# Optimization experiments

Hardware: AMD Instinct MI355X
Metric: run time of the kernel (lower is better)

## Reference

```python
import jax, jax.numpy as jnp
import numpy as np

B, T, N = 256, 2048, 64
START_IDX, END_IDX = 1, 2  # mead Offsets.GO, Offsets.EOS
NEG_INF = -10000.0


def setup_inputs() -> dict:
    key = jax.random.key(0)
    k1, k2, k3 = jax.random.split(key, 3)
    unary = jax.random.normal(k1, (B, T, N), dtype=jnp.float32)
    trans = jax.random.normal(k2, (N, N), dtype=jnp.float32) * 0.1  # [to_tag, from_tag]
    lengths = jax.random.randint(k3, (B,), T // 2, T + 1, dtype=jnp.int32)
    return {"unary": unary, "trans": trans, "lengths": lengths}


def reference(unary, trans, lengths):
    """CRF forward algorithm (partition function), batch_first input.

    unary: [B, T, N] emission scores
    trans: [N, N]    trans[j, k] = score of transitioning from tag k to tag j
    lengths: [B]     valid sequence lengths
    returns: [B]     log partition scores
    """
    unary_tbn = jnp.transpose(unary, (1, 0, 2))  # [T, B, N]
    n_tags = trans.shape[0]

    alphas0 = jnp.full((unary.shape[0], n_tags), NEG_INF, dtype=unary.dtype)
    alphas0 = alphas0.at[:, START_IDX].set(0.0)

    def step(alphas, inp):
        unary_t, t = inp  # unary_t: [B, N]
        # scores[b, j, k] = alphas[b, k] + trans[j, k] + unary_t[b, j]
        scores = alphas[:, None, :] + trans[None, :, :] + unary_t[:, :, None]
        new_alphas = jax.nn.logsumexp(scores, axis=2)  # [B, N]
        alphas = jnp.where((t < lengths)[:, None], new_alphas, alphas)
        return alphas, None

    alphas, _ = jax.lax.scan(step, alphas0, (unary_tbn, jnp.arange(T, dtype=lengths.dtype)))
    terminal = alphas + trans[END_IDX][None, :]  # transitions into EOS
    return jax.nn.logsumexp(terminal, axis=1)  # [B]
```

## Files before the change

### kernel.cpp

```cpp
#include <hip/hip_runtime.h>


typedef __attribute__((ext_vector_type(4))) float f32x4;
typedef __attribute__((ext_vector_type(8))) short bf16x8;

namespace {
constexpr int kB = 256;
constexpr int kT = 2048;
constexpr int kN = 64;
constexpr int kC = 8;
constexpr int kL = kT / kC;
constexpr int kStart = 1;
constexpr int kEnd = 2;
constexpr long kTileFloats = (long)kB * kC * 4 * 1024;
constexpr long kNumTiles = (long)kB * kC * 4;
}

__device__ __forceinline__ unsigned pack2bf(float lo, float hi) {
  return __builtin_amdgcn_perm(__float_as_uint(hi), __float_as_uint(lo), 0x07060302u);
}

__device__ __forceinline__ f32x4 expand2(unsigned u, unsigned v) {
  f32x4 e;
  e.x = __uint_as_float(u << 16);
  e.y = __uint_as_float(u & 0xFFFF0000u);
  e.z = __uint_as_float(v << 16);
  e.w = __uint_as_float(v & 0xFFFF0000u);
  return e;
}

__device__ __forceinline__ f32x4 exp4(f32x4 v) {
  f32x4 r;
  r.x = __expf(v.x);
  r.y = __expf(v.y);
  r.z = __expf(v.z);
  r.w = __expf(v.w);
  return r;
}

__device__ __forceinline__ float exp2i(int d) {
  return (d <= -127) ? 0.f : __uint_as_float((unsigned)(127 + d) << 23);
}

__device__ __forceinline__ void step64(f32x4 (&ps)[4][4], const bf16x8 (&af)[4][2],
                                       const char* lrow) {
  const f32x4 e0 = *(const f32x4*)(lrow + 0);
  const f32x4 e1 = *(const f32x4*)(lrow + 16);
  const f32x4 e2 = *(const f32x4*)(lrow + 32);
  const f32x4 e3 = *(const f32x4*)(lrow + 48);
  const f32x4 z4 = {0.f, 0.f, 0.f, 0.f};
#pragma unroll
  for (int nt = 0; nt < 4; ++nt) {
    union { unsigned u[4]; bf16x8 s; } b0u, b1u;
    b0u.u[0] = pack2bf(ps[nt][0].x, ps[nt][0].y);
    b0u.u[1] = pack2bf(ps[nt][0].z, ps[nt][0].w);
    b0u.u[2] = pack2bf(ps[nt][1].x, ps[nt][1].y);
    b0u.u[3] = pack2bf(ps[nt][1].z, ps[nt][1].w);
    b1u.u[0] = pack2bf(ps[nt][2].x, ps[nt][2].y);
    b1u.u[1] = pack2bf(ps[nt][2].z, ps[nt][2].w);
    b1u.u[2] = pack2bf(ps[nt][3].x, ps[nt][3].y);
    b1u.u[3] = pack2bf(ps[nt][3].z, ps[nt][3].w);
    const bf16x8 b0 = b0u.s, b1 = b1u.s;
    f32x4 q0 = __builtin_amdgcn_mfma_f32_16x16x32_bf16(af[0][0], b0, z4, 0, 0, 0);
    f32x4 q1 = __builtin_amdgcn_mfma_f32_16x16x32_bf16(af[1][0], b0, z4, 0, 0, 0);
    f32x4 q2 = __builtin_amdgcn_mfma_f32_16x16x32_bf16(af[2][0], b0, z4, 0, 0, 0);
    f32x4 q3 = __builtin_amdgcn_mfma_f32_16x16x32_bf16(af[3][0], b0, z4, 0, 0, 0);
    q0 = __builtin_amdgcn_mfma_f32_16x16x32_bf16(af[0][1], b1, q0, 0, 0, 0);
    q1 = __builtin_amdgcn_mfma_f32_16x16x32_bf16(af[1][1], b1, q1, 0, 0, 0);
    q2 = __builtin_amdgcn_mfma_f32_16x16x32_bf16(af[2][1], b1, q2, 0, 0, 0);
    q3 = __builtin_amdgcn_mfma_f32_16x16x32_bf16(af[3][1], b1, q3, 0, 0, 0);
    ps[nt][0] = q0 * e0;
    ps[nt][1] = q1 * e1;
    ps[nt][2] = q2 * e2;
    ps[nt][3] = q3 * e3;
  }
}

__device__ __forceinline__ void renorm64(f32x4 (&ps)[4][4], float& tot_e) {
  const unsigned eref = __builtin_amdgcn_readfirstlane(__float_as_uint(ps[0][0].x));
  const int e = (int)((eref >> 23) & 0xFFu) - 127;
  const float sc = __uint_as_float((unsigned)(127 - e) << 23);
#pragma unroll
  for (int nt = 0; nt < 4; ++nt)
#pragma unroll
    for (int mt = 0; mt < 4; ++mt) ps[nt][mt] *= sc;
  tot_e += (float)e;
}

__global__ __launch_bounds__(64, 2) void chunk64_kernel(
    const char* __restrict__ un, const float* __restrict__ trans,
    const int* __restrict__ lengths, char* __restrict__ scr, int scrStride) {
  const int b = blockIdx.x >> 3;
  const int c = blockIdx.x & 7;
  const int len = lengths[b];
  const int start = c * kL;
  int steps = len - start;
  if (steps <= 0) return;
  if (steps > kL) steps = kL;

  const int lane = threadIdx.x & 63;
  const int col = lane & 15;
  const int q4 = lane >> 4;

  bf16x8 af[4][2];
#pragma unroll
  for (int mt = 0; mt < 4; ++mt) {
#pragma unroll
    for (int kc = 0; kc < 2; ++kc) {
      union { unsigned u[4]; bf16x8 s; } fr;
#pragma unroll
      for (int jp = 0; jp < 4; ++jp) {
        const int j0 = 2 * jp, j1 = 2 * jp + 1;
        const int k0 = (2 * kc + (j0 >> 2)) * 16 + q4 * 4 + (j0 & 3);
        const int k1 = (2 * kc + (j1 >> 2)) * 16 + q4 * 4 + (j1 & 3);
        unsigned e0 = __float_as_uint(__expf(trans[(mt * 16 + col) * kN + k0])) + 0x8000u;
        unsigned e1 = __float_as_uint(__expf(trans[(mt * 16 + col) * kN + k1])) + 0x8000u;
        fr.u[jp] = __builtin_amdgcn_perm(e1, e0, 0x07060302u);
      }
      af[mt][kc] = fr.s;
    }
  }

  f32x4 ps[4][4];
#pragma unroll
  for (int nt = 0; nt < 4; ++nt) {
    const int mycol = nt * 16 + col;
#pragma unroll
    for (int mt = 0; mt < 4; ++mt) {
      const int rb = mt * 16 + q4 * 4;
      f32x4 v;
      v.x = (rb + 0 == mycol) ? 1.f : 0.f;
      v.y = (rb + 1 == mycol) ? 1.f : 0.f;
      v.z = (rb + 2 == mycol) ? 1.f : 0.f;
      v.w = (rb + 3 == mycol) ? 1.f : 0.f;
      ps[nt][mt] = v;
    }
  }

  const char* gbase = un + (size_t)(b * kT + start) * 256;
  const int srow = lane >> 2;
  const int sb = lane & 3;
  const size_t gRow = (size_t)srow * 256;

  __shared__ __align__(16) char sm[2][4096];

  {
    const char* g = gbase + gRow + sb * 16;
    f32x4 v0 = exp4(*(const f32x4*)(g + 0));
    f32x4 v1 = exp4(*(const f32x4*)(g + 64));
    f32x4 v2 = exp4(*(const f32x4*)(g + 128));
    f32x4 v3 = exp4(*(const f32x4*)(g + 192));
    char* l = &sm[0][0] + gRow + (size_t)sb * 64;
    *(f32x4*)(l + 0) = v0;
    *(f32x4*)(l + 16) = v1;
    *(f32x4*)(l + 32) = v2;
    *(f32x4*)(l + 48) = v3;
  }

  float tot_e = 0.0f;
  const int nst = (steps + 15) >> 4;
  for (int s = 0; s < nst; ++s) {
    f32x4 v0, v1, v2, v3;
    const bool more = (s + 1 < nst);
    if (more) {
      const char* g = gbase + (size_t)(s + 1) * 4096 + gRow + sb * 16;
      v0 = *(const f32x4*)(g + 0);
      v1 = *(const f32x4*)(g + 64);
      v2 = *(const f32x4*)(g + 128);
      v3 = *(const f32x4*)(g + 192);
    }

    int ns = steps - s * 16;
    ns = ns > 16 ? 16 : ns;
    const char* lb = &sm[s & 1][0] + q4 * 64;
    if (ns == 16) {
      const char* l2 = lb;
#pragma unroll 1
      for (int g4 = 0; g4 < 4; ++g4) {
        step64(ps, af, l2 + 0);
        step64(ps, af, l2 + 256);
        step64(ps, af, l2 + 512);
        step64(ps, af, l2 + 768);
        renorm64(ps, tot_e);
        l2 += 1024;
      }
    } else {
      for (int i = 0; i < ns; ++i) {
        step64(ps, af, lb + (size_t)i * 256);
        if ((i & 3) == 3) renorm64(ps, tot_e);
      }
    }

    if (more) {
      char* l = &sm[(s + 1) & 1][0] + gRow + (size_t)sb * 64;
      *(f32x4*)(l + 0) = exp4(v0);
      *(f32x4*)(l + 16) = exp4(v1);
      *(f32x4*)(l + 32) = exp4(v2);
      *(f32x4*)(l + 48) = exp4(v3);
    }
  }

  const long tbase = ((long)b * kC + c) * 4;
#pragma unroll
  for (int nt = 0; nt < 4; ++nt) {
    const long tileIdx = tbase + nt;
#pragma unroll
    for (int mt = 0; mt < 4; ++mt) {
      const long slot = tileIdx * 32 + col * 2 + (mt >> 1);
      char* addr = scr + slot * (long)scrStride + ((mt & 1) * 16 + q4 * 4) * 4;
      *(f32x4*)addr = ps[nt][mt];
    }
    if (lane == 0) {
      const long F = kTileFloats + tileIdx;
      *(float*)(scr + (F >> 5) * (long)scrStride + (F & 31) * 4) = tot_e;
    }
  }
}

__global__ __launch_bounds__(64) void combine_kernel(
    const char* __restrict__ scr, int scrStride, const float* __restrict__ trans,
    const int* __restrict__ lengths, float* __restrict__ out) {
  const int b = blockIdx.x;
  const int j = threadIdx.x;
  const int len = lengths[b];

#define LDS_SCR(F) (*(const float*)(scr + ((long)(F) >> 5) * (long)scrStride + ((F) & 31) * 4))

  const long t0 = (long)b * kC * 4;
  float a = LDS_SCR(t0 * 1024 + kStart * 64 + j);
  float totE = LDS_SCR(kTileFloats + t0);

  for (int c = 1; c < kC; ++c) {
    if (c * kL >= len) break;
    const long tb = ((long)b * kC + c) * 4;
    float s0 = 0.f, s1 = 0.f, s2 = 0.f, s3 = 0.f;
#pragma unroll
    for (int k16 = 0; k16 < 16; ++k16) {
      const float a0 = __int_as_float(__builtin_amdgcn_readlane(__float_as_int(a), k16));
      const float a1 = __int_as_float(__builtin_amdgcn_readlane(__float_as_int(a), 16 + k16));
      const float a2 = __int_as_float(__builtin_amdgcn_readlane(__float_as_int(a), 32 + k16));
      const float a3 = __int_as_float(__builtin_amdgcn_readlane(__float_as_int(a), 48 + k16));
      s0 = fmaf(LDS_SCR((tb + 0) * 1024 + k16 * 64 + j), a0, s0);
      s1 = fmaf(LDS_SCR((tb + 1) * 1024 + k16 * 64 + j), a1, s1);
      s2 = fmaf(LDS_SCR((tb + 2) * 1024 + k16 * 64 + j), a2, s2);
      s3 = fmaf(LDS_SCR((tb + 3) * 1024 + k16 * 64 + j), a3, s3);
    }
    const float e0 = LDS_SCR(kTileFloats + tb + 0);
    const float e1 = LDS_SCR(kTileFloats + tb + 1);
    const float e2 = LDS_SCR(kTileFloats + tb + 2);
    const float e3 = LDS_SCR(kTileFloats + tb + 3);
    const float em = fmaxf(fmaxf(e0, e1), fmaxf(e2, e3));
    a = s0 * exp2i((int)(e0 - em)) + s1 * exp2i((int)(e1 - em)) +
        s2 * exp2i((int)(e2 - em)) + s3 * exp2i((int)(e3 - em));
    totE += em;

    float m = a;
#pragma unroll
    for (int mask = 1; mask < 64; mask <<= 1) m = fmaxf(m, __shfl_xor(m, mask));
    const int e = (int)((__float_as_uint(m) >> 23) & 0xFFu) - 127;
    a *= exp2i(-e);
    totE += (float)e;
  }

  float term = a * __expf(trans[kEnd * kN + j]);
#pragma unroll
  for (int mask = 1; mask < 64; mask <<= 1) term += __shfl_xor(term, mask);

  if (j == 0) out[b] = totE * 0.69314718055994530942f + logf(term);
#undef LDS_SCR
}

__global__ void exp_swizzle_bf16(const float* in, char* outbase) {
  const int total = kB * kT * 32;
  int p = blockIdx.x * blockDim.x + threadIdx.x;
  const int stride = gridDim.x * blockDim.x;
  for (; p < total; p += stride) {
    const int r = p >> 5;
    const int j0 = (p & 31) << 1;
    const float2 v = *(const float2*)(in + (size_t)r * kN + j0);
    const float e0 = __expf(v.x), e1 = __expf(v.y);
    unsigned u0 = __float_as_uint(e0);
    u0 += 0x7FFFu + ((u0 >> 16) & 1u);
    unsigned u1 = __float_as_uint(e1);
    u1 += 0x7FFFu + ((u1 >> 16) & 1u);
    const unsigned d = (u1 & 0xFFFF0000u) | (u0 >> 16);
    const int pi = ((j0 >> 2) & 3) * 16 + ((j0 >> 4) << 2) + (j0 & 3);
    *(unsigned*)(outbase + (size_t)r * 256 + pi * 2) = d;
  }
}

__device__ __forceinline__ void step_lds_bf16(f32x4 (&ps)[4], const bf16x8 (&af)[4][2],
                                              const char* lrow) {
  const uint4 u0 = *(const uint4*)(lrow + 0);
  const uint4 u1 = *(const uint4*)(lrow + 16);
  f32x4 e0 = expand2(u0.x, u0.y);
  f32x4 e1 = expand2(u0.z, u0.w);
  f32x4 e2 = expand2(u1.x, u1.y);
  f32x4 e3 = expand2(u1.z, u1.w);

  union { unsigned u[4]; bf16x8 s; } b0u, b1u;
  b0u.u[0] = pack2bf(ps[0].x, ps[0].y);
  b0u.u[1] = pack2bf(ps[0].z, ps[0].w);
  b0u.u[2] = pack2bf(ps[1].x, ps[1].y);
  b0u.u[3] = pack2bf(ps[1].z, ps[1].w);
  const bf16x8 b0 = b0u.s;
  const f32x4 z4 = {0.f, 0.f, 0.f, 0.f};
  f32x4 q0 = __builtin_amdgcn_mfma_f32_16x16x32_bf16(af[0][0], b0, z4, 0, 0, 0);
  f32x4 q1 = __builtin_amdgcn_mfma_f32_16x16x32_bf16(af[1][0], b0, z4, 0, 0, 0);
  f32x4 q2 = __builtin_amdgcn_mfma_f32_16x16x32_bf16(af[2][0], b0, z4, 0, 0, 0);
  f32x4 q3 = __builtin_amdgcn_mfma_f32_16x16x32_bf16(af[3][0], b0, z4, 0, 0, 0);
  b1u.u[0] = pack2bf(ps[2].x, ps[2].y);
  b1u.u[1] = pack2bf(ps[2].z, ps[2].w);
  b1u.u[2] = pack2bf(ps[3].x, ps[3].y);
  b1u.u[3] = pack2bf(ps[3].z, ps[3].w);
  const bf16x8 b1 = b1u.s;
  q0 = __builtin_amdgcn_mfma_f32_16x16x32_bf16(af[0][1], b1, q0, 0, 0, 0);
  q1 = __builtin_amdgcn_mfma_f32_16x16x32_bf16(af[1][1], b1, q1, 0, 0, 0);
  q2 = __builtin_amdgcn_mfma_f32_16x16x32_bf16(af[2][1], b1, q2, 0, 0, 0);
  q3 = __builtin_amdgcn_mfma_f32_16x16x32_bf16(af[3][1], b1, q3, 0, 0, 0);

  ps[0] = q0 * e0;
  ps[1] = q1 * e1;
  ps[2] = q2 * e2;
  ps[3] = q3 * e3;
}

__device__ __forceinline__ void renorm16(f32x4 (&ps)[4], float& tot_e) {
  const unsigned eref = __builtin_amdgcn_readfirstlane(__float_as_uint(ps[0].x));
  const int e = (int)((eref >> 23) & 0xFFu) - 127;
  const float sc = __uint_as_float((unsigned)(127 - e) << 23);
#pragma unroll
  for (int mt = 0; mt < 4; ++mt) ps[mt] *= sc;
  tot_e += (float)e;
}

__global__ __launch_bounds__(256, 3) void chunk_pair_bf16_kernel(
    const char* __restrict__ eu, const float* __restrict__ trans,
    const int* __restrict__ lengths, char* __restrict__ scr, int scrStride) {
  constexpr int RB = 128;
  constexpr int SEG = RB / 8;
  constexpr int STG = 32 * RB;

  const int b = blockIdx.x >> 2;
  const int cp = blockIdx.x & 3;
  const int len = lengths[b];
  const int cA = 2 * cp, cB = 2 * cp + 1;
  int stepsA = len - cA * kL;
  stepsA = stepsA < 0 ? 0 : (stepsA > kL ? kL : stepsA);
  int stepsB = len - cB * kL;
  stepsB = stepsB < 0 ? 0 : (stepsB > kL ? kL : stepsB);
  if (stepsA <= 0) return;

  const int t8 = threadIdx.x;
  const int lane = t8 & 63;
  const int w = t8 >> 6;
  const int col = lane & 15;
  const int q4 = lane >> 4;

  bf16x8 af[4][2];
#pragma unroll
  for (int mt = 0; mt < 4; ++mt) {
#pragma unroll
    for (int kc = 0; kc < 2; ++kc) {
      union { unsigned u[4]; bf16x8 s; } fr;
#pragma unroll
      for (int jp = 0; jp < 4; ++jp) {
        const int j0 = 2 * jp, j1 = 2 * jp + 1;
        const int k0 = (2 * kc + (j0 >> 2)) * 16 + q4 * 4 + (j0 & 3);
        const int k1 = (2 * kc + (j1 >> 2)) * 16 + q4 * 4 + (j1 & 3);
        unsigned e0 = __float_as_uint(__expf(trans[(mt * 16 + col) * kN + k0])) + 0x8000u;
        unsigned e1 = __float_as_uint(__expf(trans[(mt * 16 + col) * kN + k1])) + 0x8000u;
        fr.u[jp] = __builtin_amdgcn_perm(e1, e0, 0x07060302u);
      }
      af[mt][kc] = fr.s;
    }
  }

  const int mycol = w * 16 + col;
  f32x4 psA[4], psB[4];
#pragma unroll
  for (int mt = 0; mt < 4; ++mt) {
    const int rb = mt * 16 + q4 * 4;
    f32x4 v;
    v.x = (rb + 0 == mycol) ? 1.f : 0.f;
    v.y = (rb + 1 == mycol) ? 1.f : 0.f;
    v.z = (rb + 2 == mycol) ? 1.f : 0.f;
    v.w = (rb + 3 == mycol) ? 1.f : 0.f;
    psA[mt] = v;
    psB[mt] = v;
  }

  const char* gblkA = eu + (size_t)(b * kT + cA * kL) * 256;
  const char* gblkB = eu + (size_t)(b * kT + cB * kL) * 256;
  const size_t gOff = (size_t)(t8 >> 3) * 256 + (size_t)(t8 & 7) * SEG;
  const size_t lOff = (size_t)(t8 >> 3) * RB + (size_t)(t8 & 7) * SEG;

  __shared__ __align__(16) char smem[2][2][STG];

  {
    uint4 vaA = *(const uint4*)(gblkA + gOff);
    uint4 vaB = *(const uint4*)(gblkB + gOff);
    *(uint4*)(&smem[0][0][0] + lOff) = vaA;
    *(uint4*)(&smem[1][0][0] + lOff) = vaB;
  }
  __syncthreads();

  float totA = 0.0f, totB = 0.0f;
  for (int s = 0; s < 8; ++s) {
    uint4 vaA, vaB;
    const bool more = (s < 7);
    if (more) {
      vaA = *(const uint4*)(gblkA + (size_t)(s + 1) * 8192 + gOff);
      vaB = *(const uint4*)(gblkB + (size_t)(s + 1) * 8192 + gOff);
    }

    int nsA = stepsA - s * 32;
    nsA = nsA < 0 ? 0 : (nsA > 32 ? 32 : nsA);
    int nsB = stepsB - s * 32;
    nsB = nsB < 0 ? 0 : (nsB > 32 ? 32 : nsB);
    const char* lbA = &smem[0][s & 1][0] + q4 * (RB / 4);
    const char* lbB = &smem[1][s & 1][0] + q4 * (RB / 4);

    if (nsA == 32 && nsB == 32) {
      for (int g = 0; g < 8; ++g) {
#pragma unroll
        for (int k = 0; k < 4; ++k) {
          step_lds_bf16(psA, af, lbA + (g * 4 + k) * RB);
          step_lds_bf16(psB, af, lbB + (g * 4 + k) * RB);
        }
        renorm16(psA, totA);
        renorm16(psB, totB);
      }
    } else {
      for (int i = 0; i < nsA; ++i) {
        step_lds_bf16(psA, af, lbA + (size_t)i * RB);
        if ((i & 3) == 3) renorm16(psA, totA);
      }
      for (int i = 0; i < nsB; ++i) {
        step_lds_bf16(psB, af, lbB + (size_t)i * RB);
        if ((i & 3) == 3) renorm16(psB, totB);
      }
    }

    if (more) {
      *(uint4*)(&smem[0][(s + 1) & 1][0] + lOff) = vaA;
      *(uint4*)(&smem[1][(s + 1) & 1][0] + lOff) = vaB;
    }
    __syncthreads();
  }

  {
    const long tileIdx = ((long)b * kC + cA) * 4 + w;
#pragma unroll
    for (int mt = 0; mt < 4; ++mt) {
      const long slot = tileIdx * 32 + col * 2 + (mt >> 1);
      char* addr = scr + slot * (long)scrStride + ((mt & 1) * 16 + q4 * 4) * 4;
      *(f32x4*)addr = psA[mt];
    }
    if (lane == 0) {
      const long F = kTileFloats + tileIdx;
      *(float*)(scr + (F >> 5) * (long)scrStride + (F & 31) * 4) = totA;
    }
  }
  if (stepsB > 0) {
    const long tileIdx = ((long)b * kC + cB) * 4 + w;
#pragma unroll
    for (int mt = 0; mt < 4; ++mt) {
      const long slot = tileIdx * 32 + col * 2 + (mt >> 1);
      char* addr = scr + slot * (long)scrStride + ((mt & 1) * 16 + q4 * 4) * 4;
      *(f32x4*)addr = psB[mt];
    }
    if (lane == 0) {
      const long F = kTileFloats + tileIdx;
      *(float*)(scr + (F >> 5) * (long)scrStride + (F & 31) * 4) = totB;
    }
  }
}

extern "C" void kernel_launch(void* const* d_in, const int* in_sizes, int n_in,
                              void* d_out, int out_size, void* d_ws, size_t ws_size,
                              hipStream_t stream) {
  const float* unary = (const float*)d_in[0];
  const float* trans = (const float*)d_in[1];
  const int* lengths = (const int*)d_in[2];
  float* out = (float*)d_out;

  const size_t scrBytes = (size_t)(kTileFloats + kNumTiles) * 4;

  if (ws_size >= scrBytes) {
    chunk64_kernel<<<dim3(kB * kC), dim3(64), 0, stream>>>(
        (const char*)d_in[0], trans, lengths, (char*)d_ws, 128);
    combine_kernel<<<dim3(kB), dim3(64), 0, stream>>>((const char*)d_ws, 128,
                                                      trans, lengths, out);
  } else {
    exp_swizzle_bf16<<<dim3(4096), dim3(256), 0, stream>>>(unary, (char*)d_in[0]);
    chunk_pair_bf16_kernel<<<dim3(kB * 4), dim3(256), 0, stream>>>(
        (const char*)d_in[0], trans, lengths, (char*)d_in[0] + 128, 256);
    combine_kernel<<<dim3(kB), dim3(64), 0, stream>>>((const char*)d_in[0] + 128,
                                                      256, trans, lengths, out);
  }
}
```

Before: 410.3 us.

## Split chunk kernel columns across two waves and prefetch combine matrices

Each chunk's 64 identity columns are now split across two blocks of 32 columns, doubling the grid to 4096 single-wave blocks. Each block carries half the MFMA work per step, which shortens the serial chain per wave and raises occupancy (launch bounds now 3). The cost is that each block loads and exponentiates the same unary tile on its own, doubling that work. The combine kernel also prefetches the next chunk's transfer matrix into registers while computing the current one, and fully unrolls the chunk loop, at the price of higher register pressure.

```diff
diff --git a/kernel.cpp b/kernel.cpp
--- a/kernel.cpp
+++ b/kernel.cpp
@@ -42,7 +42,11 @@
   return (d <= -127) ? 0.f : __uint_as_float((unsigned)(127 + d) << 23);
 }
 
-__device__ __forceinline__ void step64(f32x4 (&ps)[4][4], const bf16x8 (&af)[4][2],
+__device__ __forceinline__ float scr_rd(const char* scr, int scrStride, long F) {
+  return *(const float*)(scr + (F >> 5) * (long)scrStride + (F & 31) * 4);
+}
+
+__device__ __forceinline__ void step32(f32x4 (&ps)[2][4], const bf16x8 (&af)[4][2],
                                        const char* lrow) {
   const f32x4 e0 = *(const f32x4*)(lrow + 0);
   const f32x4 e1 = *(const f32x4*)(lrow + 16);
@@ -50,7 +54,7 @@
   const f32x4 e3 = *(const f32x4*)(lrow + 48);
   const f32x4 z4 = {0.f, 0.f, 0.f, 0.f};
 #pragma unroll
-  for (int nt = 0; nt < 4; ++nt) {
+  for (int nt = 0; nt < 2; ++nt) {
     union { unsigned u[4]; bf16x8 s; } b0u, b1u;
     b0u.u[0] = pack2bf(ps[nt][0].x, ps[nt][0].y);
     b0u.u[1] = pack2bf(ps[nt][0].z, ps[nt][0].w);
@@ -76,22 +80,24 @@
   }
 }
 
-__device__ __forceinline__ void renorm64(f32x4 (&ps)[4][4], float& tot_e) {
+__device__ __forceinline__ void renorm32(f32x4 (&ps)[2][4], float& tot_e) {
   const unsigned eref = __builtin_amdgcn_readfirstlane(__float_as_uint(ps[0][0].x));
   const int e = (int)((eref >> 23) & 0xFFu) - 127;
   const float sc = __uint_as_float((unsigned)(127 - e) << 23);
 #pragma unroll
-  for (int nt = 0; nt < 4; ++nt)
+  for (int nt = 0; nt < 2; ++nt)
 #pragma unroll
     for (int mt = 0; mt < 4; ++mt) ps[nt][mt] *= sc;
   tot_e += (float)e;
 }
 
-__global__ __launch_bounds__(64, 2) void chunk64_kernel(
+__global__ __launch_bounds__(64, 3) void chunk32_kernel(
     const char* __restrict__ un, const float* __restrict__ trans,
     const int* __restrict__ lengths, char* __restrict__ scr, int scrStride) {
-  const int b = blockIdx.x >> 3;
-  const int c = blockIdx.x & 7;
+  const int bid = blockIdx.x;
+  const int b = bid >> 4;
+  const int c = (bid >> 1) & 7;
+  const int h = bid & 1;
   const int len = lengths[b];
   const int start = c * kL;
   int steps = len - start;
@@ -121,10 +127,10 @@
     }
   }
 
-  f32x4 ps[4][4];
-#pragma unroll
-  for (int nt = 0; nt < 4; ++nt) {
-    const int mycol = nt * 16 + col;
+  f32x4 ps[2][4];
+#pragma unroll
+  for (int nt = 0; nt < 2; ++nt) {
+    const int mycol = h * 32 + nt * 16 + col;
 #pragma unroll
     for (int mt = 0; mt < 4; ++mt) {
       const int rb = mt * 16 + q4 * 4;
@@ -177,17 +183,17 @@
       const char* l2 = lb;
 #pragma unroll 1
       for (int g4 = 0; g4 < 4; ++g4) {
-        step64(ps, af, l2 + 0);
-        step64(ps, af, l2 + 256);
-        step64(ps, af, l2 + 512);
-        step64(ps, af, l2 + 768);
-        renorm64(ps, tot_e);
+        step32(ps, af, l2 + 0);
+        step32(ps, af, l2 + 256);
+        step32(ps, af, l2 + 512);
+        step32(ps, af, l2 + 768);
+        renorm32(ps, tot_e);
         l2 += 1024;
       }
     } else {
       for (int i = 0; i < ns; ++i) {
-        step64(ps, af, lb + (size_t)i * 256);
-        if ((i & 3) == 3) renorm64(ps, tot_e);
+        step32(ps, af, lb + (size_t)i * 256);
+        if ((i & 3) == 3) renorm32(ps, tot_e);
       }
     }
 
@@ -200,9 +206,9 @@
     }
   }
 
-  const long tbase = ((long)b * kC + c) * 4;
-#pragma unroll
-  for (int nt = 0; nt < 4; ++nt) {
+  const long tbase = ((long)b * kC + c) * 4 + h * 2;
+#pragma unroll
+  for (int nt = 0; nt < 2; ++nt) {
     const long tileIdx = tbase + nt;
 #pragma unroll
     for (int mt = 0; mt < 4; ++mt) {
@@ -217,49 +223,71 @@
   }
 }
 
-__global__ __launch_bounds__(64) void combine_kernel(
+__device__ __forceinline__ void load_mat(const char* scr, int scrStride, long tb,
+                                         int j, float (&m)[4][16], float (&ev)[4]) {
+#pragma unroll
+  for (int s = 0; s < 4; ++s) {
+#pragma unroll
+    for (int k = 0; k < 16; ++k)
+      m[s][k] = scr_rd(scr, scrStride, (tb + s) * 1024 + (long)k * 64 + j);
+    ev[s] = scr_rd(scr, scrStride, kTileFloats + tb + s);
+  }
+}
+
+__global__ __launch_bounds__(64, 1) void combine_kernel(
     const char* __restrict__ scr, int scrStride, const float* __restrict__ trans,
     const int* __restrict__ lengths, float* __restrict__ out) {
   const int b = blockIdx.x;
   const int j = threadIdx.x;
   const int len = lengths[b];
 
-#define LDS_SCR(F) (*(const float*)(scr + ((long)(F) >> 5) * (long)scrStride + ((F) & 31) * 4))
-
   const long t0 = (long)b * kC * 4;
-  float a = LDS_SCR(t0 * 1024 + kStart * 64 + j);
-  float totE = LDS_SCR(kTileFloats + t0);
-
+  float a = scr_rd(scr, scrStride, t0 * 1024 + kStart * 64 + j);
+  float totE = scr_rd(scr, scrStride, kTileFloats + t0);
+
+  float mc[4][16], ec[4];
+  load_mat(scr, scrStride, t0 + 4, j, mc, ec);
+
+#pragma unroll
   for (int c = 1; c < kC; ++c) {
-    if (c * kL >= len) break;
-    const long tb = ((long)b * kC + c) * 4;
-    float s0 = 0.f, s1 = 0.f, s2 = 0.f, s3 = 0.f;
-#pragma unroll
-    for (int k16 = 0; k16 < 16; ++k16) {
-      const float a0 = __int_as_float(__builtin_amdgcn_readlane(__float_as_int(a), k16));
-      const float a1 = __int_as_float(__builtin_amdgcn_readlane(__float_as_int(a), 16 + k16));
-      const float a2 = __int_as_float(__builtin_amdgcn_readlane(__float_as_int(a), 32 + k16));
-      const float a3 = __int_as_float(__builtin_amdgcn_readlane(__float_as_int(a), 48 + k16));
-      s0 = fmaf(LDS_SCR((tb + 0) * 1024 + k16 * 64 + j), a0, s0);
-      s1 = fmaf(LDS_SCR((tb + 1) * 1024 + k16 * 64 + j), a1, s1);
-      s2 = fmaf(LDS_SCR((tb + 2) * 1024 + k16 * 64 + j), a2, s2);
-      s3 = fmaf(LDS_SCR((tb + 3) * 1024 + k16 * 64 + j), a3, s3);
-    }
-    const float e0 = LDS_SCR(kTileFloats + tb + 0);
-    const float e1 = LDS_SCR(kTileFloats + tb + 1);
-    const float e2 = LDS_SCR(kTileFloats + tb + 2);
-    const float e3 = LDS_SCR(kTileFloats + tb + 3);
-    const float em = fmaxf(fmaxf(e0, e1), fmaxf(e2, e3));
-    a = s0 * exp2i((int)(e0 - em)) + s1 * exp2i((int)(e1 - em)) +
-        s2 * exp2i((int)(e2 - em)) + s3 * exp2i((int)(e3 - em));
-    totE += em;
-
-    float m = a;
-#pragma unroll
-    for (int mask = 1; mask < 64; mask <<= 1) m = fmaxf(m, __shfl_xor(m, mask));
-    const int e = (int)((__float_as_uint(m) >> 23) & 0xFFu) - 127;
-    a *= exp2i(-e);
-    totE += (float)e;
+    float mn[4][16], en[4];
+    if (c + 1 < kC)
+      load_mat(scr, scrStride, t0 + (long)(c + 1) * 4, j, mn, en);
+
+    if (c * kL < len) {
+      float s0 = 0.f, s1 = 0.f, s2 = 0.f, s3 = 0.f;
+#pragma unroll
+      for (int k16 = 0; k16 < 16; ++k16) {
+        const float a0 = __int_as_float(__builtin_amdgcn_readlane(__float_as_int(a), k16));
+        const float a1 = __int_as_float(__builtin_amdgcn_readlane(__float_as_int(a), 16 + k16));
+        const float a2 = __int_as_float(__builtin_amdgcn_readlane(__float_as_int(a), 32 + k16));
+        const float a3 = __int_as_float(__builtin_amdgcn_readlane(__float_as_int(a), 48 + k16));
+        s0 = fmaf(mc[0][k16], a0, s0);
+        s1 = fmaf(mc[1][k16], a1, s1);
+        s2 = fmaf(mc[2][k16], a2, s2);
+        s3 = fmaf(mc[3][k16], a3, s3);
+      }
+      const float em = fmaxf(fmaxf(ec[0], ec[1]), fmaxf(ec[2], ec[3]));
+      a = s0 * exp2i((int)(ec[0] - em)) + s1 * exp2i((int)(ec[1] - em)) +
+          s2 * exp2i((int)(ec[2] - em)) + s3 * exp2i((int)(ec[3] - em));
+      totE += em;
+
+      float m = a;
+#pragma unroll
+      for (int mask = 1; mask < 64; mask <<= 1) m = fmaxf(m, __shfl_xor(m, mask));
+      const int e = (int)((__float_as_uint(m) >> 23) & 0xFFu) - 127;
+      a *= exp2i(-e);
+      totE += (float)e;
+    }
+
+    if (c + 1 < kC) {
+#pragma unroll
+      for (int s = 0; s < 4; ++s) {
+#pragma unroll
+        for (int k = 0; k < 16; ++k) mc[s][k] = mn[s][k];
+        ec[s] = en[s];
+      }
+    }
   }
 
   float term = a * __expf(trans[kEnd * kN + j]);
@@ -267,7 +295,6 @@
   for (int mask = 1; mask < 64; mask <<= 1) term += __shfl_xor(term, mask);
 
   if (j == 0) out[b] = totE * 0.69314718055994530942f + logf(term);
-#undef LDS_SCR
 }
 
 __global__ void exp_swizzle_bf16(const float* in, char* outbase) {
@@ -488,7 +515,7 @@
   const size_t scrBytes = (size_t)(kTileFloats + kNumTiles) * 4;
 
   if (ws_size >= scrBytes) {
-    chunk64_kernel<<<dim3(kB * kC), dim3(64), 0, stream>>>(
+    chunk32_kernel<<<dim3(kB * kC * 2), dim3(64), 0, stream>>>(
         (const char*)d_in[0], trans, lengths, (char*)d_ws, 128);
     combine_kernel<<<dim3(kB), dim3(64), 0, stream>>>((const char*)d_ws, 128,
                                                       trans, lengths, out);
```

After: 391.8 us. 1.05x faster.
